# Kernel optimization log

Measured on AMD Instinct MI355X. Metric: run time of the kernel, lower is better.

## Reference

```python
import jax, jax.numpy as jnp
import numpy as np

E = 100000    # number of edges
T = 1000000   # number of triplets
D = 128       # embed_dim
NB = 20       # n_basis (angle expansion width)
EPS = 1e-6


def setup_inputs() -> dict:
    key = jax.random.key(0)
    ks = jax.random.split(key, 14)
    def lin(k, fan_in, fan_out):
        # torch.nn.Linear default init: U(-1/sqrt(fan_in), 1/sqrt(fan_in))
        bound = 1.0 / np.sqrt(fan_in)
        kw, kb = jax.random.split(k)
        W = jax.random.uniform(kw, (fan_in, fan_out), jnp.float32, -bound, bound)
        b = jax.random.uniform(kb, (fan_out,), jnp.float32, -bound, bound)
        return W, b
    edge_attr = jax.random.normal(ks[0], (E, D), jnp.float32)
    edge_vectors = jax.random.normal(ks[1], (E, 3), jnp.float32)
    three_body_indices = jax.random.randint(ks[2], (T, 3), 0, 50000, jnp.int64)
    three_body_edge_indices = jax.random.randint(ks[3], (T, 2), 0, E, jnp.int64)
    Wa1, ba1 = lin(ks[4], 3, NB)          # SimpleMLPAngleExpansion layer 1
    Wa2, ba2 = lin(ks[5], NB, NB)         # SimpleMLPAngleExpansion layer 2
    W1, b1 = lin(ks[6], 2 * D + NB, D)    # phi_3b layer 1
    W2, b2 = lin(ks[7], D, D)             # phi_3b layer 2
    Wu, bu = lin(ks[8], D, D)             # update_edge
    return {
        "edge_attr": edge_attr,
        "three_body_indices": three_body_indices,
        "three_body_edge_indices": three_body_edge_indices,
        "edge_vectors": edge_vectors,
        "Wa1": Wa1, "ba1": ba1, "Wa2": Wa2, "ba2": ba2,
        "W1": W1, "b1": b1, "W2": W2, "b2": b2,
        "Wu": Wu, "bu": bu,
    }


def reference(edge_attr, three_body_indices, three_body_edge_indices, edge_vectors,
              Wa1, ba1, Wa2, ba2, W1, b1, W2, b2, Wu, bu):
    e_ij = three_body_edge_indices[:, 0]
    e_ik = three_body_edge_indices[:, 1]
    # gather edge vectors for the two edges forming the angle (sign-flipped)
    vec_ij = -edge_vectors[e_ij]           # (T, 3)
    vec_ik = -edge_vectors[e_ik]           # (T, 3)
    len_ij = jnp.maximum(jnp.linalg.norm(vec_ij, axis=1, keepdims=True), EPS)
    len_ik = jnp.maximum(jnp.linalg.norm(vec_ik, axis=1, keepdims=True), EPS)
    cos_t = jnp.clip(jnp.sum(vec_ij * vec_ik, axis=1, keepdims=True) / (len_ij * len_ik), -1.0, 1.0)
    # SimpleMLPAngleExpansion: (T,3) -> (T, NB)
    ang_in = jnp.concatenate([len_ij, len_ik, cos_t], axis=-1)
    angle_feats = jax.nn.silu(ang_in @ Wa1 + ba1) @ Wa2 + ba2
    # triplet features: gathered edge embeddings + angle features
    h_3b = jnp.concatenate([edge_attr[e_ij], edge_attr[e_ik], angle_feats], axis=-1)  # (T, 2D+NB)
    h_3b = jnp.nan_to_num(h_3b, nan=0.0, posinf=0.0, neginf=0.0)
    # phi_3b: Linear -> SiLU -> Linear
    m_ijk = jax.nn.silu(h_3b @ W1 + b1) @ W2 + b2   # (T, D)
    # scatter-add messages back to edge ij
    delta = jax.ops.segment_sum(m_ijk, e_ij, num_segments=edge_attr.shape[0])  # (E, D)
    return jnp.nan_to_num(delta @ Wu + bu, nan=0.0, posinf=0.0, neginf=0.0)
```

## Files before the change

kernel.cpp:

```cpp
#include <hip/hip_runtime.h>
#include <stdint.h>

#define NB 20
#define EG 8

typedef __attribute__((ext_vector_type(8))) short bf16x8;
typedef __attribute__((ext_vector_type(4))) float f32x4;

__device__ __forceinline__ float bf_lo(uint32_t u) { return __uint_as_float(u << 16); }
__device__ __forceinline__ float bf_hi(uint32_t u) { return __uint_as_float(u & 0xffff0000u); }
__device__ __forceinline__ uint32_t f2bf(float f) {
    uint32_t u = __float_as_uint(f);
    return (u + 0x7fffu + ((u >> 16) & 1u)) >> 16;
}
__device__ __forceinline__ uint32_t pack_bf2(float a, float b) {
    return f2bf(a) | (f2bf(b) << 16);
}
__device__ __forceinline__ float silu_f(float x) {
    float e = __builtin_amdgcn_exp2f(-1.4426950408889634f * x);
    return x * __builtin_amdgcn_rcpf(1.f + e);
}

__global__ void __launch_bounds__(256) prepA(const float* __restrict__ W2,
                                             const float* __restrict__ b2,
                                             const float* __restrict__ Wu,
                                             const float* __restrict__ W1,
                                             float* __restrict__ Mf32,
                                             float* __restrict__ cvec,
                                             uint32_t* __restrict__ Bpk) {
    const int bid = blockIdx.x, tid = threadIdx.x;
    if (bid < 65) {
        int k = bid * 2 + (tid >> 7);
        int col = tid & 127;
        if (k <= 128) {
            const float* row = (k < 128) ? (W2 + k * 128) : b2;
            float acc = 0.f;
            for (int j = 0; j < 128; ++j) acc = fmaf(row[j], Wu[j * 128 + col], acc);
            if (k < 128) Mf32[k * 128 + col] = acc;
            else cvec[col] = acc;
        }
    } else {
        int d = (bid - 65) * 256 + tid;
        int q = d & 3, l = (d >> 2) & 63, c = (d >> 8) & 15, s = d >> 12;
        int k = 32 * s + ((l >> 4) << 3) + (q << 1);
        int col = (c << 4) + (l & 15);
        int r0 = (col < 128) ? k : (k + 128);
        int cc = col & 127;
        float v0 = W1[(size_t)r0 * 128 + cc];
        float v1 = W1[(size_t)(r0 + 1) * 128 + cc];
        Bpk[d] = pack_bf2(v0, v1);
    }
}

__global__ void prepM(const float* __restrict__ Mf32, uint32_t* __restrict__ Mfrag) {
    int d = blockIdx.x * 256 + threadIdx.x;
    int q = d & 3, l = (d >> 2) & 63, c = (d >> 8) & 7, s = d >> 11;
    int k = 32 * s + ((l >> 4) << 3) + (q << 1);
    int col = (c << 4) + (l & 15);
    Mfrag[d] = pack_bf2(Mf32[k * 128 + col], Mf32[(k + 1) * 128 + col]);
}

__global__ void __launch_bounds__(256) kA3(const float* __restrict__ edge_attr,
                                           const uint32_t* __restrict__ Bpk,
                                           uint16_t* __restrict__ Pb, int E) {
    __shared__ uint32_t As[4096];
    __shared__ uint32_t Bs[16384];
    const int tid = threadIdx.x;
    const int e0 = blockIdx.x * 64;
    const int nE = min(64, E - e0);

    for (int d = tid; d < 4096; d += 256) {
        int row = d >> 6, p = d & 63;
        int g = p >> 2;
        float2 v;
        if (row < nE) v = *(const float2*)(edge_attr + (size_t)(e0 + row) * 128 + 2 * p);
        else { v.x = 0.f; v.y = 0.f; }
        As[row * 64 + ((g ^ (row & 7)) << 2) + (p & 3)] = pack_bf2(v.x, v.y);
    }
    for (int d = tid; d < 4096; d += 256)
        ((uint4*)Bs)[d] = ((const uint4*)Bpk)[d];
    __syncthreads();

    const int w = tid >> 6, l = tid & 63;

    bf16x8 afr[4][4];
#pragma unroll
    for (int rb = 0; rb < 4; ++rb)
#pragma unroll
        for (int s = 0; s < 4; ++s) {
            int row = rb * 16 + (l & 15);
            int g = s * 4 + (l >> 4);
            afr[rb][s] = *(const bf16x8*)((const char*)As + row * 256 + ((g ^ (row & 7)) << 4));
        }

    f32x4 acc[4][4];
#pragma unroll
    for (int cl = 0; cl < 4; ++cl)
#pragma unroll
        for (int rb = 0; rb < 4; ++rb) acc[cl][rb] = (f32x4)(0.f);

#pragma unroll
    for (int cl = 0; cl < 4; ++cl) {
        const int c = w * 4 + cl;
#pragma unroll
        for (int s = 0; s < 4; ++s) {
            bf16x8 bfr = *(const bf16x8*)((const char*)Bs + (((s * 16 + c) * 64 + l) << 4));
#pragma unroll
            for (int rb = 0; rb < 4; ++rb)
                acc[cl][rb] = __builtin_amdgcn_mfma_f32_16x16x32_bf16(afr[rb][s], bfr, acc[cl][rb], 0, 0, 0);
        }
    }

#pragma unroll
    for (int cl = 0; cl < 4; ++cl)
#pragma unroll
        for (int rb = 0; rb < 4; ++rb)
#pragma unroll
            for (int r = 0; r < 4; ++r) {
                int row = rb * 16 + (l >> 4) * 4 + r;
                if (row < nE)
                    Pb[(size_t)(e0 + row) * 256 + w * 64 + cl * 16 + (l & 15)] = (uint16_t)f2bf(acc[cl][rb][r]);
            }
}

__global__ void khist(const int* __restrict__ tbe, uint32_t* __restrict__ cnt, int T) {
    int t = blockIdx.x * blockDim.x + threadIdx.x;
    int stride = gridDim.x * blockDim.x;
    int half = T >> 1;
    for (; t < half; t += stride) {
        int4 ee = ((const int4*)tbe)[t];
        atomicAdd(&cnt[ee.x], 1u);
        atomicAdd(&cnt[ee.z], 1u);
    }
}

__global__ void scanA(const uint32_t* __restrict__ cnt, uint32_t* __restrict__ bsum, int E) {
    __shared__ uint32_t s[256];
    int tid = threadIdx.x;
    int e = blockIdx.x * 256 + tid;
    s[tid] = (e < E) ? cnt[e] : 0u;
    __syncthreads();
    for (int off = 128; off > 0; off >>= 1) {
        if (tid < off) s[tid] += s[tid + off];
        __syncthreads();
    }
    if (tid == 0) bsum[blockIdx.x] = s[0];
}

__global__ void scanB(uint32_t* __restrict__ bsum, int n) {
    __shared__ uint32_t s[512];
    int tid = threadIdx.x;
    s[tid] = (tid < n) ? bsum[tid] : 0u;
    __syncthreads();
    for (int off = 1; off < 512; off <<= 1) {
        uint32_t a = (tid >= off) ? s[tid - off] : 0u;
        __syncthreads();
        s[tid] += a;
        __syncthreads();
    }
    if (tid < n) bsum[tid] = (tid > 0) ? s[tid - 1] : 0u;
}

__global__ void scanC(const uint32_t* __restrict__ cnt, const uint32_t* __restrict__ bsum,
                      uint32_t* __restrict__ offs, int E) {
    __shared__ uint32_t s[256];
    int tid = threadIdx.x;
    int e = blockIdx.x * 256 + tid;
    uint32_t v = (e < E) ? cnt[e] : 0u;
    s[tid] = v;
    __syncthreads();
    for (int off = 1; off < 256; off <<= 1) {
        uint32_t a = (tid >= off) ? s[tid - off] : 0u;
        __syncthreads();
        s[tid] += a;
        __syncthreads();
    }
    if (e < E) offs[e] = bsum[blockIdx.x] + s[tid] - v;
}

__global__ void __launch_bounds__(256) kSA(const int* __restrict__ tbe,
                                           const float* __restrict__ evec,
                                           const float* __restrict__ Wa1,
                                           const float* __restrict__ ba1,
                                           const float* __restrict__ Wa2,
                                           const float* __restrict__ ba2,
                                           uint32_t* __restrict__ offs,
                                           uint32_t* __restrict__ afpk,
                                           uint32_t* __restrict__ sortedE2, int T) {
    __shared__ float wa1_s[60], ba1_s[NB], wa2_s[400], ba2_s[NB];
    const int tid = threadIdx.x;
    for (int i = tid; i < 400; i += 256) wa2_s[i] = Wa2[i];
    if (tid < 60) wa1_s[tid] = Wa1[tid];
    if (tid < NB) { ba1_s[tid] = ba1[tid]; ba2_s[tid] = ba2[tid]; }
    __syncthreads();

    const int t = blockIdx.x * 256 + tid;
    if (t >= T) return;

    int2 ee = ((const int2*)tbe)[t];
    const float ax = evec[ee.x * 3], ay = evec[ee.x * 3 + 1], az = evec[ee.x * 3 + 2];
    const float bx = evec[ee.y * 3], by = evec[ee.y * 3 + 1], bz = evec[ee.y * 3 + 2];
    const float li = fmaxf(__builtin_amdgcn_sqrtf(ax * ax + ay * ay + az * az), 1e-6f);
    const float lk = fmaxf(__builtin_amdgcn_sqrtf(bx * bx + by * by + bz * bz), 1e-6f);
    float ct = (ax * bx + ay * by + az * bz) * __builtin_amdgcn_rcpf(li * lk);
    ct = fminf(fmaxf(ct, -1.f), 1.f);

    float h[NB];
#pragma unroll
    for (int o = 0; o < NB; ++o) {
        float z = fmaf(li, wa1_s[o], fmaf(lk, wa1_s[20 + o], fmaf(ct, wa1_s[40 + o], ba1_s[o])));
        h[o] = silu_f(z);
    }
    float af[NB];
#pragma unroll
    for (int o2 = 0; o2 < NB; ++o2) af[o2] = ba2_s[o2];
#pragma unroll
    for (int o = 0; o < NB; ++o) {
#pragma unroll
        for (int o2 = 0; o2 < NB; ++o2) af[o2] = fmaf(h[o], wa2_s[o * 20 + o2], af[o2]);
    }

    const uint32_t pos = atomicAdd(&offs[ee.x], 1u);
    sortedE2[pos] = (uint32_t)ee.y;
    uint32_t* dst = afpk + (size_t)pos * 10;
#pragma unroll
    for (int j = 0; j < 5; ++j) {
        uint2 pk;
        pk.x = pack_bf2(af[4 * j], af[4 * j + 1]);
        pk.y = pack_bf2(af[4 * j + 2], af[4 * j + 3]);
        *(uint2*)(dst + 2 * j) = pk;
    }
}

__global__ void __launch_bounds__(256) kB7(const uint32_t* __restrict__ sortedE2,
                                           const uint32_t* __restrict__ offs,
                                           const float* __restrict__ W1,
                                           const float* __restrict__ b1,
                                           const uint32_t* __restrict__ Ppk,
                                           const uint32_t* __restrict__ afpk,
                                           float* __restrict__ S, int E) {
    __shared__ __align__(16) float af_s[4][64 * 20];
    __shared__ uint32_t e2_s[4][64];

    const int tid = threadIdx.x;
    const int wave = tid >> 6, lane = tid & 63;
    const int gw = blockIdx.x * 4 + wave;
    const int eb = gw * EG;
    if (eb >= E) return;
    const int ee = min(eb + EG, E);

    uint32_t offv = 0u;
    {
        int oi = eb - 1 + lane;
        if (lane <= EG && oi >= 0) offv = offs[min(oi, E - 1)];
    }
    const uint32_t tstart = __shfl(offv, 0);
    const uint32_t tend = __shfl(offv, ee - eb);

    float2 wreg[NB];
#pragma unroll
    for (int k = 0; k < NB; ++k)
        wreg[k] = *(const float2*)(W1 + (size_t)(256 + k) * 128 + 2 * lane);
    const float2 b1v = ((const float2*)b1)[lane];

    int ecur = eb;
    uint32_t eend = __shfl(offv, 1);
    uint32_t p1A = Ppk[(size_t)ecur * 128 + lane];
    uint32_t p1B = Ppk[(size_t)min(ecur + 1, E - 1) * 128 + lane];
    float p1lo = bf_lo(p1A) + b1v.x;
    float p1hi = bf_hi(p1A) + b1v.y;
    float acc0 = 0.f, acc1 = 0.f;

    float* afw = af_s[wave];

    for (uint32_t base = tstart; base < tend; base += 64u) {
        const int m = min(64, (int)(tend - base));
        const uint32_t idx = min(base + (uint32_t)lane, tend - 1u);
        e2_s[wave][lane] = sortedE2[idx];
        const uint32_t base10 = base * 10u;
        for (int i = lane; i < m * 10; i += 64) {
            const uint32_t u = afpk[base10 + i];
            afw[2 * i] = bf_lo(u);
            afw[2 * i + 1] = bf_hi(u);
        }
        asm volatile("s_waitcnt lgkmcnt(0)" ::: "memory");
        __builtin_amdgcn_sched_barrier(0);

        uint32_t p2a = Ppk[(size_t)e2_s[wave][0] * 128 + 64 + lane];
        uint32_t p2b = (m > 1) ? Ppk[(size_t)e2_s[wave][1] * 128 + 64 + lane] : p2a;
        int i2 = 0;
        while (i2 < m) {
            const uint32_t rem = eend - base;
            const int lim = (rem < (uint32_t)m) ? (int)rem : m;
            for (; i2 < lim; ++i2) {
                const uint32_t p2 = p2a;
                p2a = p2b;
                if (i2 + 2 < m) p2b = Ppk[(size_t)e2_s[wave][i2 + 2] * 128 + 64 + lane];
                float x0 = p1lo + bf_lo(p2);
                float x1 = p1hi + bf_hi(p2);
                const float4* afp = (const float4*)(afw + i2 * 20);
                const float4 fA = afp[0], fB = afp[1], fC = afp[2], fD = afp[3], fE = afp[4];
                const float a_[20] = {fA.x, fA.y, fA.z, fA.w, fB.x, fB.y, fB.z, fB.w,
                                      fC.x, fC.y, fC.z, fC.w, fD.x, fD.y, fD.z, fD.w,
                                      fE.x, fE.y, fE.z, fE.w};
#pragma unroll
                for (int j = 0; j < NB; ++j) {
                    x0 = fmaf(a_[j], wreg[j].x, x0);
                    x1 = fmaf(a_[j], wreg[j].y, x1);
                }
                acc0 += silu_f(x0);
                acc1 += silu_f(x1);
            }
            if (base + (uint32_t)i2 == eend) {
                do {
                    float2 o;
                    o.x = acc0;
                    o.y = acc1;
                    ((float2*)S)[(size_t)ecur * 64 + lane] = o;
                    acc0 = 0.f;
                    acc1 = 0.f;
                    ++ecur;
                    if (ecur >= ee) { eend = 0xffffffffu; break; }
                    p1A = p1B;
                    p1B = Ppk[(size_t)min(ecur + 1, E - 1) * 128 + lane];
                    p1lo = bf_lo(p1A) + b1v.x;
                    p1hi = bf_hi(p1A) + b1v.y;
                    eend = __shfl(offv, ecur - eb + 1);
                } while (base + (uint32_t)i2 == eend);
            }
        }
    }
    while (ecur < ee) {
        float2 o;
        o.x = acc0;
        o.y = acc1;
        ((float2*)S)[(size_t)ecur * 64 + lane] = o;
        acc0 = 0.f;
        acc1 = 0.f;
        ++ecur;
    }
}

__global__ void __launch_bounds__(256) kC2(const float* __restrict__ S,
                                           const uint32_t* __restrict__ Mfrag,
                                           const float* __restrict__ cvec,
                                           const float* __restrict__ bu,
                                           const uint32_t* __restrict__ cnt,
                                           int E) {
    __shared__ uint32_t As[4096];
    __shared__ uint32_t Bs[8192];
    __shared__ float cnt_s[64];
    const int tid = threadIdx.x;
    const int e0 = blockIdx.x * 64;
    const int nE = min(64, E - e0);

    for (int d = tid; d < 4096; d += 256) {
        int row = d >> 6, p = d & 63;
        int g = p >> 2;
        float2 v;
        if (row < nE) v = *(const float2*)(S + (size_t)(e0 + row) * 128 + 2 * p);
        else { v.x = 0.f; v.y = 0.f; }
        As[row * 64 + ((g ^ (row & 7)) << 2) + (p & 3)] = pack_bf2(v.x, v.y);
    }
    for (int d = tid; d < 2048; d += 256)
        ((uint4*)Bs)[d] = ((const uint4*)Mfrag)[d];
    if (tid < 64) cnt_s[tid] = (tid < nE) ? (float)cnt[e0 + tid] : 0.f;
    __syncthreads();

    const int w = tid >> 6, l = tid & 63;

    bf16x8 afr[4][4];
#pragma unroll
    for (int rb = 0; rb < 4; ++rb)
#pragma unroll
        for (int s = 0; s < 4; ++s) {
            int row = rb * 16 + (l & 15);
            int g = s * 4 + (l >> 4);
            afr[rb][s] = *(const bf16x8*)((const char*)As + row * 256 + ((g ^ (row & 7)) << 4));
        }

    f32x4 acc[2][4];
#pragma unroll
    for (int cl = 0; cl < 2; ++cl)
#pragma unroll
        for (int rb = 0; rb < 4; ++rb) acc[cl][rb] = (f32x4)(0.f);

#pragma unroll
    for (int cl = 0; cl < 2; ++cl) {
        const int c = w * 2 + cl;
#pragma unroll
        for (int s = 0; s < 4; ++s) {
            bf16x8 bfr = *(const bf16x8*)((const char*)Bs + (((s * 8 + c) * 64 + l) << 4));
#pragma unroll
            for (int rb = 0; rb < 4; ++rb)
                acc[cl][rb] = __builtin_amdgcn_mfma_f32_16x16x32_bf16(afr[rb][s], bfr, acc[cl][rb], 0, 0, 0);
        }
    }

#pragma unroll
    for (int cl = 0; cl < 2; ++cl) {
        const int col = w * 32 + cl * 16 + (l & 15);
        const float cv = cvec[col];
        const float bv = bu[col];
#pragma unroll
        for (int rb = 0; rb < 4; ++rb)
#pragma unroll
            for (int r = 0; r < 4; ++r) {
                int row = rb * 16 + (l >> 4) * 4 + r;
                if (row < nE) {
                    float* dst = (float*)S + (size_t)(e0 + row) * 128 + col;
                    *dst = acc[cl][rb][r] + fmaf(cnt_s[row], cv, bv);
                }
            }
    }
}

extern "C" void kernel_launch(void* const* d_in, const int* in_sizes, int n_in,
                              void* d_out, int out_size, void* d_ws, size_t ws_size,
                              hipStream_t stream) {
    const float* edge_attr = (const float*)d_in[0];
    const int* tbe = (const int*)d_in[2];
    const float* evec = (const float*)d_in[3];
    const float* Wa1 = (const float*)d_in[4];
    const float* ba1 = (const float*)d_in[5];
    const float* Wa2 = (const float*)d_in[6];
    const float* ba2 = (const float*)d_in[7];
    const float* W1 = (const float*)d_in[8];
    const float* b1 = (const float*)d_in[9];
    const float* W2 = (const float*)d_in[10];
    const float* b2 = (const float*)d_in[11];
    const float* Wu = (const float*)d_in[12];
    const float* bu = (const float*)d_in[13];

    const int E = in_sizes[0] / 128;
    const int T = in_sizes[2] / 2;
    float* S = (float*)d_out;

    const int nScanBlk = (E + 255) / 256;

    char* ws = (char*)d_ws;
    size_t off = 0;
    uint32_t* Ppk = (uint32_t*)(ws + off); off += (size_t)E * 512;
    uint32_t* cnt = (uint32_t*)(ws + off); off += (size_t)E * 4;
    uint32_t* offs = (uint32_t*)(ws + off); off += (size_t)E * 4;
    uint32_t* sortedE2 = (uint32_t*)(ws + off); off += (size_t)T * 4;
    uint32_t* afpk = (uint32_t*)(ws + off); off += (size_t)T * 40;
    uint32_t* bsum = (uint32_t*)(ws + off); off += (size_t)((nScanBlk + 3) & ~3) * 4;
    uint32_t* Bpk = (uint32_t*)(ws + off); off += 65536;
    float* Mf32 = (float*)(ws + off); off += 65536;
    uint32_t* Mfrag = (uint32_t*)(ws + off); off += 32768;
    float* cvec = (float*)(ws + off); off += 512;

    hipMemsetAsync(cnt, 0, (size_t)E * 4, stream);

    prepA<<<129, 256, 0, stream>>>(W2, b2, Wu, W1, Mf32, cvec, Bpk);
    prepM<<<32, 256, 0, stream>>>(Mf32, Mfrag);
    kA3<<<(E + 63) / 64, 256, 0, stream>>>(edge_attr, Bpk, (uint16_t*)Ppk, E);
    khist<<<1024, 256, 0, stream>>>(tbe, cnt, T);
    scanA<<<nScanBlk, 256, 0, stream>>>(cnt, bsum, E);
    scanB<<<1, 512, 0, stream>>>(bsum, nScanBlk);
    scanC<<<nScanBlk, 256, 0, stream>>>(cnt, bsum, offs, E);
    kSA<<<(T + 255) / 256, 256, 0, stream>>>(tbe, evec, Wa1, ba1, Wa2, ba2,
                                             offs, afpk, sortedE2, T);
    const int nWaves = (E + EG - 1) / EG;
    kB7<<<(nWaves + 3) / 4, 256, 0, stream>>>(sortedE2, offs, W1, b1, Ppk, afpk, S, E);
    kC2<<<(E + 63) / 64, 256, 0, stream>>>(S, Mfrag, cvec, bu, cnt, E);
}
```

Baseline: 497.9 us.

## Use packed fp16 dot2 for angle-feature projection and fuse prepM into prepA

Angle features and the angle rows of W1 are now stored as packed fp16 pairs. The per-triplet inner loop uses v_dot2 (fdot2) instead of 20 scalar FMAs per output, and the angle features stay packed in LDS rather than being unpacked to fp32, which halves LDS traffic per triplet. The separate prepM launch is folded into prepA through shared memory, and the staging buffers are padded so unconditional vector loads stay in bounds. This trades a small amount of precision (fp16 round-toward-zero) for fewer VALU and LDS operations in the hot kernel.

```diff
diff --git a/kernel.cpp b/kernel.cpp
--- a/kernel.cpp
+++ b/kernel.cpp
@@ -6,6 +6,7 @@
 
 typedef __attribute__((ext_vector_type(8))) short bf16x8;
 typedef __attribute__((ext_vector_type(4))) float f32x4;
+typedef _Float16 h16x2 __attribute__((ext_vector_type(2)));
 
 __device__ __forceinline__ float bf_lo(uint32_t u) { return __uint_as_float(u << 16); }
 __device__ __forceinline__ float bf_hi(uint32_t u) { return __uint_as_float(u & 0xffff0000u); }
@@ -16,6 +17,9 @@
 __device__ __forceinline__ uint32_t pack_bf2(float a, float b) {
     return f2bf(a) | (f2bf(b) << 16);
 }
+__device__ __forceinline__ uint32_t pack_h2(float a, float b) {
+    return __builtin_bit_cast(uint32_t, __builtin_amdgcn_cvt_pkrtz(a, b));
+}
 __device__ __forceinline__ float silu_f(float x) {
     float e = __builtin_amdgcn_exp2f(-1.4426950408889634f * x);
     return x * __builtin_amdgcn_rcpf(1.f + e);
@@ -25,21 +29,34 @@
                                              const float* __restrict__ b2,
                                              const float* __restrict__ Wu,
                                              const float* __restrict__ W1,
-                                             float* __restrict__ Mf32,
                                              float* __restrict__ cvec,
-                                             uint32_t* __restrict__ Bpk) {
+                                             uint32_t* __restrict__ Bpk,
+                                             uint32_t* __restrict__ W1cf16,
+                                             uint32_t* __restrict__ Mfrag) {
     const int bid = blockIdx.x, tid = threadIdx.x;
     if (bid < 65) {
-        int k = bid * 2 + (tid >> 7);
-        int col = tid & 127;
+        __shared__ float mrow[2][128];
+        const int half = tid >> 7;
+        const int k = bid * 2 + half;
+        const int col = tid & 127;
+        float acc = 0.f;
         if (k <= 128) {
             const float* row = (k < 128) ? (W2 + k * 128) : b2;
-            float acc = 0.f;
             for (int j = 0; j < 128; ++j) acc = fmaf(row[j], Wu[j * 128 + col], acc);
-            if (k < 128) Mf32[k * 128 + col] = acc;
-            else cvec[col] = acc;
-        }
-    } else {
+        }
+        if (k == 128) cvec[col] = acc;
+        mrow[half][col] = acc;
+        __syncthreads();
+        if (bid < 64 && half == 0) {
+            const int kk = bid * 2;
+            const int s = kk >> 5;
+            const int lhi = (kk & 31) >> 3;
+            const int q = (kk & 7) >> 1;
+            const int c = col >> 4;
+            const int l = (lhi << 4) | (col & 15);
+            Mfrag[((s * 8 + c) * 64 + l) * 4 + q] = pack_bf2(mrow[0][col], mrow[1][col]);
+        }
+    } else if (bid < 129) {
         int d = (bid - 65) * 256 + tid;
         int q = d & 3, l = (d >> 2) & 63, c = (d >> 8) & 15, s = d >> 12;
         int k = 32 * s + ((l >> 4) << 3) + (q << 1);
@@ -49,15 +66,14 @@
         float v0 = W1[(size_t)r0 * 128 + cc];
         float v1 = W1[(size_t)(r0 + 1) * 128 + cc];
         Bpk[d] = pack_bf2(v0, v1);
-    }
-}
-
-__global__ void prepM(const float* __restrict__ Mf32, uint32_t* __restrict__ Mfrag) {
-    int d = blockIdx.x * 256 + threadIdx.x;
-    int q = d & 3, l = (d >> 2) & 63, c = (d >> 8) & 7, s = d >> 11;
-    int k = 32 * s + ((l >> 4) << 3) + (q << 1);
-    int col = (c << 4) + (l & 15);
-    Mfrag[d] = pack_bf2(Mf32[k * 128 + col], Mf32[(k + 1) * 128 + col]);
+    } else {
+        for (int d = tid; d < 1280; d += 256) {
+            int j2 = d >> 7, c = d & 127;
+            float v0 = W1[(size_t)(256 + 2 * j2) * 128 + c];
+            float v1 = W1[(size_t)(257 + 2 * j2) * 128 + c];
+            W1cf16[d] = pack_h2(v0, v1);
+        }
+    }
 }
 
 __global__ void __launch_bounds__(256) kA3(const float* __restrict__ edge_attr,
@@ -226,20 +242,20 @@
 #pragma unroll
     for (int j = 0; j < 5; ++j) {
         uint2 pk;
-        pk.x = pack_bf2(af[4 * j], af[4 * j + 1]);
-        pk.y = pack_bf2(af[4 * j + 2], af[4 * j + 3]);
+        pk.x = pack_h2(af[4 * j], af[4 * j + 1]);
+        pk.y = pack_h2(af[4 * j + 2], af[4 * j + 3]);
         *(uint2*)(dst + 2 * j) = pk;
     }
 }
 
-__global__ void __launch_bounds__(256) kB7(const uint32_t* __restrict__ sortedE2,
+__global__ void __launch_bounds__(256) kB8(const uint32_t* __restrict__ sortedE2,
                                            const uint32_t* __restrict__ offs,
-                                           const float* __restrict__ W1,
+                                           const uint32_t* __restrict__ W1cf16,
                                            const float* __restrict__ b1,
                                            const uint32_t* __restrict__ Ppk,
                                            const uint32_t* __restrict__ afpk,
                                            float* __restrict__ S, int E) {
-    __shared__ __align__(16) float af_s[4][64 * 20];
+    __shared__ __align__(8) uint32_t af_s[4][64 * 10];
     __shared__ uint32_t e2_s[4][64];
 
     const int tid = threadIdx.x;
@@ -257,10 +273,13 @@
     const uint32_t tstart = __shfl(offv, 0);
     const uint32_t tend = __shfl(offv, ee - eb);
 
-    float2 wreg[NB];
-#pragma unroll
-    for (int k = 0; k < NB; ++k)
-        wreg[k] = *(const float2*)(W1 + (size_t)(256 + k) * 128 + 2 * lane);
+    h16x2 wx[10], wy[10];
+#pragma unroll
+    for (int j = 0; j < 10; ++j) {
+        uint2 w2 = *(const uint2*)(W1cf16 + j * 128 + 2 * lane);
+        wx[j] = __builtin_bit_cast(h16x2, w2.x);
+        wy[j] = __builtin_bit_cast(h16x2, w2.y);
+    }
     const float2 b1v = ((const float2*)b1)[lane];
 
     int ecur = eb;
@@ -271,17 +290,25 @@
     float p1hi = bf_hi(p1A) + b1v.y;
     float acc0 = 0.f, acc1 = 0.f;
 
-    float* afw = af_s[wave];
+    uint32_t* afw = af_s[wave];
 
     for (uint32_t base = tstart; base < tend; base += 64u) {
         const int m = min(64, (int)(tend - base));
         const uint32_t idx = min(base + (uint32_t)lane, tend - 1u);
         e2_s[wave][lane] = sortedE2[idx];
-        const uint32_t base10 = base * 10u;
-        for (int i = lane; i < m * 10; i += 64) {
-            const uint32_t u = afpk[base10 + i];
-            afw[2 * i] = bf_lo(u);
-            afw[2 * i + 1] = bf_hi(u);
+        {
+            const uint32_t* src = afpk + ((size_t)base + (uint32_t)lane) * 10u;
+            uint32_t* dst = afw + lane * 10;
+            uint2 s0 = *(const uint2*)(src);
+            uint2 s1 = *(const uint2*)(src + 2);
+            uint2 s2 = *(const uint2*)(src + 4);
+            uint2 s3 = *(const uint2*)(src + 6);
+            uint2 s4 = *(const uint2*)(src + 8);
+            *(uint2*)(dst) = s0;
+            *(uint2*)(dst + 2) = s1;
+            *(uint2*)(dst + 4) = s2;
+            *(uint2*)(dst + 6) = s3;
+            *(uint2*)(dst + 8) = s4;
         }
         asm volatile("s_waitcnt lgkmcnt(0)" ::: "memory");
         __builtin_amdgcn_sched_barrier(0);
@@ -296,17 +323,21 @@
                 const uint32_t p2 = p2a;
                 p2a = p2b;
                 if (i2 + 2 < m) p2b = Ppk[(size_t)e2_s[wave][i2 + 2] * 128 + 64 + lane];
+                const uint32_t* afp = afw + i2 * 10;
+                uint2 u0 = *(const uint2*)(afp);
+                uint2 u1 = *(const uint2*)(afp + 2);
+                uint2 u2 = *(const uint2*)(afp + 4);
+                uint2 u3 = *(const uint2*)(afp + 6);
+                uint2 u4 = *(const uint2*)(afp + 8);
+                const uint32_t aw[10] = {u0.x, u0.y, u1.x, u1.y, u2.x,
+                                         u2.y, u3.x, u3.y, u4.x, u4.y};
                 float x0 = p1lo + bf_lo(p2);
                 float x1 = p1hi + bf_hi(p2);
-                const float4* afp = (const float4*)(afw + i2 * 20);
-                const float4 fA = afp[0], fB = afp[1], fC = afp[2], fD = afp[3], fE = afp[4];
-                const float a_[20] = {fA.x, fA.y, fA.z, fA.w, fB.x, fB.y, fB.z, fB.w,
-                                      fC.x, fC.y, fC.z, fC.w, fD.x, fD.y, fD.z, fD.w,
-                                      fE.x, fE.y, fE.z, fE.w};
-#pragma unroll
-                for (int j = 0; j < NB; ++j) {
-                    x0 = fmaf(a_[j], wreg[j].x, x0);
-                    x1 = fmaf(a_[j], wreg[j].y, x1);
+#pragma unroll
+                for (int j = 0; j < 10; ++j) {
+                    h16x2 ah = __builtin_bit_cast(h16x2, aw[j]);
+                    x0 = __builtin_amdgcn_fdot2(ah, wx[j], x0, false);
+                    x1 = __builtin_amdgcn_fdot2(ah, wy[j], x1, false);
                 }
                 acc0 += silu_f(x0);
                 acc1 += silu_f(x1);
@@ -443,18 +474,17 @@
     uint32_t* Ppk = (uint32_t*)(ws + off); off += (size_t)E * 512;
     uint32_t* cnt = (uint32_t*)(ws + off); off += (size_t)E * 4;
     uint32_t* offs = (uint32_t*)(ws + off); off += (size_t)E * 4;
-    uint32_t* sortedE2 = (uint32_t*)(ws + off); off += (size_t)T * 4;
-    uint32_t* afpk = (uint32_t*)(ws + off); off += (size_t)T * 40;
+    uint32_t* sortedE2 = (uint32_t*)(ws + off); off += ((size_t)T + 64) * 4;
+    uint32_t* afpk = (uint32_t*)(ws + off); off += ((size_t)T + 64) * 40;
     uint32_t* bsum = (uint32_t*)(ws + off); off += (size_t)((nScanBlk + 3) & ~3) * 4;
     uint32_t* Bpk = (uint32_t*)(ws + off); off += 65536;
-    float* Mf32 = (float*)(ws + off); off += 65536;
+    uint32_t* W1cf16 = (uint32_t*)(ws + off); off += 8192;
     uint32_t* Mfrag = (uint32_t*)(ws + off); off += 32768;
     float* cvec = (float*)(ws + off); off += 512;
 
     hipMemsetAsync(cnt, 0, (size_t)E * 4, stream);
 
-    prepA<<<129, 256, 0, stream>>>(W2, b2, Wu, W1, Mf32, cvec, Bpk);
-    prepM<<<32, 256, 0, stream>>>(Mf32, Mfrag);
+    prepA<<<130, 256, 0, stream>>>(W2, b2, Wu, W1, cvec, Bpk, W1cf16, Mfrag);
     kA3<<<(E + 63) / 64, 256, 0, stream>>>(edge_attr, Bpk, (uint16_t*)Ppk, E);
     khist<<<1024, 256, 0, stream>>>(tbe, cnt, T);
     scanA<<<nScanBlk, 256, 0, stream>>>(cnt, bsum, E);
@@ -463,6 +493,6 @@
     kSA<<<(T + 255) / 256, 256, 0, stream>>>(tbe, evec, Wa1, ba1, Wa2, ba2,
                                              offs, afpk, sortedE2, T);
     const int nWaves = (E + EG - 1) / EG;
-    kB7<<<(nWaves + 3) / 4, 256, 0, stream>>>(sortedE2, offs, W1, b1, Ppk, afpk, S, E);
+    kB8<<<(nWaves + 3) / 4, 256, 0, stream>>>(sortedE2, offs, W1cf16, b1, Ppk, afpk, S, E);
     kC2<<<(E + 63) / 64, 256, 0, stream>>>(S, Mfrag, cvec, bu, cnt, E);
 }
```

Result: faster. 463.5 us (-6.9%).
